# Performance work log

Measured on AMD Instinct MI355X. Metric: run time of the kernel, lower is better.

## Reference

```python
import jax, jax.numpy as jnp
import numpy as np

C = 345  # class_num


def setup_inputs() -> dict:
    key = jax.random.key(0)
    k1, k2, k3, k4, k5, k6, k7 = jax.random.split(key, 7)
    N, A = 128, 512
    fc_weight = jax.random.normal(k1, (C, A), dtype=jnp.float32) * 0.02
    features_source = jax.random.normal(k2, (N, A), dtype=jnp.float32)
    y_s = jax.random.normal(k3, (N, C), dtype=jnp.float32)
    labels_source = jax.random.randint(k4, (N,), 0, C, dtype=jnp.int64)
    mean_source = jax.random.normal(k5, (C, A), dtype=jnp.float32) * 0.1
    mean_target = jax.random.normal(k6, (C, A), dtype=jnp.float32) * 0.1
    covariance_target = jax.random.normal(k7, (C, A, A), dtype=jnp.float32) * 0.01
    Lambda = jnp.float32(0.5)
    return {
        "fc_weight": fc_weight,
        "features_source": features_source,
        "y_s": y_s,
        "labels_source": labels_source,
        "Lambda": Lambda,
        "mean_source": mean_source,
        "mean_target": mean_target,
        "covariance_target": covariance_target,
    }


def _aug(fc_weight, y_s, labels_s, Lambda, mean_source, mean_target, covariance_target):
    # NxW_ij = weight broadcast to [N,C,A]; NxW_kj = weight[labels] broadcast over C.
    # dataW[n,c,:] = W[c] - W[labels[n]]   -> [N,C,A]
    W_lbl = fc_weight[labels_s]                       # [N,A]
    dataW = fc_weight[None, :, :] - W_lbl[:, None, :]  # [N,C,A]

    Sigma = covariance_target[labels_s]               # [N,A,A]
    # diag of (dataW @ Sigma @ dataW^T): einsum directly for the diagonal
    tmp = jnp.einsum('nca,nab->ncb', dataW, Sigma)    # [N,C,A]
    sigma2 = Lambda * jnp.einsum('nca,nca->nc', tmp, dataW)  # [N,C]

    dMean = mean_target[labels_s] - mean_source[labels_s]   # [N,A]
    dW_dMean = jnp.einsum('nca,na->nc', dataW, dMean)        # [N,C]

    return y_s + 0.5 * sigma2 + Lambda * dW_dMean


def reference(fc_weight, features_source, y_s, labels_source, Lambda,
              mean_source, mean_target, covariance_target):
    aug_y = _aug(fc_weight, y_s, labels_source, Lambda,
                 mean_source, mean_target, covariance_target)
    logp = jax.nn.log_softmax(aug_y, axis=-1)
    N = aug_y.shape[0]
    nll = -logp[jnp.arange(N), labels_source]
    return jnp.mean(nll)
```

## Files before the change

kernel.cpp:

```cpp
#include <hip/hip_runtime.h>
#include <hip/hip_bf16.h>
#include <math.h>

#define C_NUM 345
#define A_DIM 512
#define N_NUM 128
#define KB    128
#define NBB   4

typedef short bf16x8 __attribute__((ext_vector_type(8)));
typedef float f32x4  __attribute__((ext_vector_type(4)));

__device__ __forceinline__ short f2bf(float f) {
    unsigned u = __builtin_bit_cast(unsigned, f);
    u += 0x7fffu + ((u >> 16) & 1u);
    return (short)(u >> 16);
}

__device__ __forceinline__ int swz(int r, int k) {
    return r * 128 + ((((k >> 3) ^ (r & 15)) << 3) | (k & 7));
}

__global__ __launch_bounds__(256, 2) void qkern(
    const float* __restrict__ W,
    const int*   __restrict__ labels,
    const float* __restrict__ cov,
    float*       __restrict__ q2)
{
    const int bb = blockIdx.x;
    const int n  = blockIdx.y;
    const int b0 = bb * KB;
    const int l  = labels[n];
    const float* __restrict__ Sg = cov + (size_t)l * A_DIM * A_DIM;
    const float* __restrict__ Wl = W + (size_t)l * A_DIM;

    __shared__ short Sa[128 * 128];
    __shared__ short Vb[128 * 128];

    const int tid  = threadIdx.x;
    const int lane = tid & 63;
    const int w    = tid >> 6;
    const int wa   = w & 1;
    const int wc   = w >> 1;
    const int l15  = lane & 15;
    const int g    = lane >> 4;

    const int c4 = tid & 31;
    const int r0 = tid >> 5;

    const float4 wl4 = *(const float4*)(Wl + b0 + c4 * 4);

    float qp[3][4];
#pragma unroll
    for (int ct = 0; ct < 3; ct++)
#pragma unroll
        for (int j = 0; j < 4; j++) qp[ct][j] = 0.f;

    for (int at = 0; at < A_DIM; at += 128) {
        float4 wle[4];
#pragma unroll
        for (int i = 0; i < 4; i++)
            wle[i] = *(const float4*)(Wl + at + wa * 64 + i * 16 + g * 4);

        for (int ct = 0; ct < 3; ct++) {
            __syncthreads();
            if (ct == 0) {
#pragma unroll
                for (int p = 0; p < 16; p++) {
                    const int r = r0 + p * 8;
                    const float4 s = *(const float4*)(Sg + (size_t)(at + r) * A_DIM + b0 + c4 * 4);
                    short4 h = make_short4(f2bf(s.x), f2bf(s.y), f2bf(s.z), f2bf(s.w));
                    *(short4*)(&Sa[swz(r, c4 * 4)]) = h;
                }
            }
#pragma unroll
            for (int p = 0; p < 16; p++) {
                const int r = r0 + p * 8;
                const int c = ct * 128 + r;
                short4 h;
                if (c < C_NUM) {
                    const float4 wv = *(const float4*)(W + (size_t)c * A_DIM + b0 + c4 * 4);
                    h = make_short4(f2bf(wv.x - wl4.x), f2bf(wv.y - wl4.y),
                                    f2bf(wv.z - wl4.z), f2bf(wv.w - wl4.w));
                } else {
                    h = make_short4(0, 0, 0, 0);
                }
                *(short4*)(&Vb[swz(r, c4 * 4)]) = h;
            }
            __syncthreads();

            f32x4 acc[4][4];
#pragma unroll
            for (int i = 0; i < 4; i++)
#pragma unroll
                for (int j = 0; j < 4; j++) {
                    f32x4 z = {0.f, 0.f, 0.f, 0.f};
                    acc[i][j] = z;
                }

#pragma unroll
            for (int kt = 0; kt < 4; kt++) {
                const int kbase = kt * 32 + g * 8;
                bf16x8 af[4], bfr[4];
#pragma unroll
                for (int i = 0; i < 4; i++)
                    af[i] = *(const bf16x8*)(&Sa[swz(wa * 64 + i * 16 + l15, kbase)]);
#pragma unroll
                for (int j = 0; j < 4; j++)
                    bfr[j] = *(const bf16x8*)(&Vb[swz(wc * 64 + j * 16 + l15, kbase)]);
#pragma unroll
                for (int i = 0; i < 4; i++)
#pragma unroll
                    for (int j = 0; j < 4; j++)
                        acc[i][j] = __builtin_amdgcn_mfma_f32_16x16x32_bf16(
                            af[i], bfr[j], acc[i][j], 0, 0, 0);
            }

#pragma unroll
            for (int i = 0; i < 4; i++) {
                const int a0 = at + wa * 64 + i * 16 + g * 4;
                const float4 wl_e = wle[i];
#pragma unroll
                for (int j = 0; j < 4; j++) {
                    const int c = ct * 128 + wc * 64 + j * 16 + l15;
                    if (c < C_NUM) {
                        const float4 wv = *(const float4*)(W + (size_t)c * A_DIM + a0);
                        const f32x4 u = acc[i][j];
                        qp[ct][j] += u[0] * (wv.x - wl_e.x) + u[1] * (wv.y - wl_e.y)
                                   + u[2] * (wv.z - wl_e.z) + u[3] * (wv.w - wl_e.w);
                    }
                }
            }
        }
    }

#pragma unroll
    for (int ct = 0; ct < 3; ct++)
#pragma unroll
        for (int j = 0; j < 4; j++) {
            float v = qp[ct][j];
            v += __shfl_xor(v, 16);
            v += __shfl_xor(v, 32);
            if (g == 0) {
                const int c = ct * 128 + wc * 64 + j * 16 + l15;
                if (c < C_NUM) atomicAdd(&q2[(size_t)n * C_NUM + c], v);
            }
        }
}

__global__ __launch_bounds__(256) void losskern(
    const float* __restrict__ W,
    const float* __restrict__ ys,
    const int*   __restrict__ labels,
    const float* __restrict__ lambda_p,
    const float* __restrict__ mean_s,
    const float* __restrict__ mean_t,
    const float* __restrict__ q2,
    float*       __restrict__ out)
{
    const int n = blockIdx.x;
    const int tid = threadIdx.x;
    const int lane = tid & 63;
    const int w = tid >> 6;
    const int l = labels[n];
    const float Lam = *lambda_p;

    __shared__ float aug[C_NUM];
    __shared__ float red[256];

    const int a0 = lane * 8;
    const float* Wl = W + (size_t)l * A_DIM;
    const float4 wl0 = *(const float4*)(Wl + a0);
    const float4 wl1 = *(const float4*)(Wl + a0 + 4);
    const float4 mt0 = *(const float4*)(mean_t + (size_t)l * A_DIM + a0);
    const float4 mt1 = *(const float4*)(mean_t + (size_t)l * A_DIM + a0 + 4);
    const float4 ms0 = *(const float4*)(mean_s + (size_t)l * A_DIM + a0);
    const float4 ms1 = *(const float4*)(mean_s + (size_t)l * A_DIM + a0 + 4);
    const float dm0 = mt0.x - ms0.x, dm1 = mt0.y - ms0.y, dm2 = mt0.z - ms0.z, dm3 = mt0.w - ms0.w;
    const float dm4 = mt1.x - ms1.x, dm5 = mt1.y - ms1.y, dm6 = mt1.z - ms1.z, dm7 = mt1.w - ms1.w;
    const float wldm = wl0.x*dm0 + wl0.y*dm1 + wl0.z*dm2 + wl0.w*dm3
                     + wl1.x*dm4 + wl1.y*dm5 + wl1.z*dm6 + wl1.w*dm7;

    for (int c = w; c < C_NUM; c += 4) {
        const float* Wc = W + (size_t)c * A_DIM;
        const float4 w0 = *(const float4*)(Wc + a0);
        const float4 w1 = *(const float4*)(Wc + a0 + 4);
        float d = w0.x*dm0 + w0.y*dm1 + w0.z*dm2 + w0.w*dm3
                + w1.x*dm4 + w1.y*dm5 + w1.z*dm6 + w1.w*dm7 - wldm;
        d += __shfl_xor(d, 1);
        d += __shfl_xor(d, 2);
        d += __shfl_xor(d, 4);
        d += __shfl_xor(d, 8);
        d += __shfl_xor(d, 16);
        d += __shfl_xor(d, 32);
        if (lane == 0)
            aug[c] = ys[(size_t)n * C_NUM + c] + 0.5f * Lam * q2[(size_t)n * C_NUM + c] + Lam * d;
    }
    __syncthreads();

    float m = -INFINITY;
    for (int c = tid; c < C_NUM; c += 256) m = fmaxf(m, aug[c]);
    red[tid] = m;
    __syncthreads();
    for (int s = 128; s > 0; s >>= 1) {
        if (tid < s) red[tid] = fmaxf(red[tid], red[tid + s]);
        __syncthreads();
    }
    m = red[0];
    __syncthreads();

    float se = 0.f;
    for (int c = tid; c < C_NUM; c += 256) se += expf(aug[c] - m);
    red[tid] = se;
    __syncthreads();
    for (int s = 128; s > 0; s >>= 1) {
        if (tid < s) red[tid] += red[tid + s];
        __syncthreads();
    }
    if (tid == 0) {
        const float logZ = m + logf(red[0]);
        atomicAdd(out, (logZ - aug[l]) * (1.f / (float)N_NUM));
    }
}

extern "C" void kernel_launch(void* const* d_in, const int* in_sizes, int n_in,
                              void* d_out, int out_size, void* d_ws, size_t ws_size,
                              hipStream_t stream) {
    const float* W      = (const float*)d_in[0];
    const float* ys     = (const float*)d_in[2];
    const int*   labels = (const int*)d_in[3];
    const float* lam    = (const float*)d_in[4];
    const float* means  = (const float*)d_in[5];
    const float* meant  = (const float*)d_in[6];
    const float* cov    = (const float*)d_in[7];
    float* out = (float*)d_out;
    float* q2  = (float*)d_ws;

    hipMemsetAsync(q2, 0, (size_t)N_NUM * C_NUM * sizeof(float), stream);
    hipMemsetAsync(out, 0, sizeof(float), stream);

    qkern<<<dim3(NBB, N_NUM), 256, 0, stream>>>(W, labels, cov, q2);
    losskern<<<N_NUM, 256, 0, stream>>>(W, ys, labels, lam, means, meant, q2, out);
}
```

Before: 555.2 us.

## Keep full W-difference tile resident in LDS and double-buffer covariance tiles

The quadratic-form kernel now uses 64-wide b-chunks over 8 blocks per sample. For each chunk it loads the whole padded 384-row weight-difference tile into shared memory once, instead of rebuilding it for every class tile and every a-tile. Covariance tiles are register-prefetched for the next a-step and written into a double-buffered shared array, so global loads overlap the MFMA work and only one barrier is needed per step. This removes repeated W conversions and cuts synchronisation. In exchange it doubles the grid and increases accumulator register pressure (4x6 MFMA tiles per wave).

After: 573.4 us. +3.3%, slower.

```diff
diff --git a/kernel.cpp b/kernel.cpp
--- a/kernel.cpp
+++ b/kernel.cpp
@@ -3,10 +3,11 @@
 #include <math.h>
 
 #define C_NUM 345
+#define CP    384
 #define A_DIM 512
 #define N_NUM 128
-#define KB    128
-#define NBB   4
+#define KB    64
+#define NBB   8
 
 typedef short bf16x8 __attribute__((ext_vector_type(8)));
 typedef float f32x4  __attribute__((ext_vector_type(4)));
@@ -17,8 +18,8 @@
     return (short)(u >> 16);
 }
 
-__device__ __forceinline__ int swz(int r, int k) {
-    return r * 128 + ((((k >> 3) ^ (r & 15)) << 3) | (k & 7));
+__device__ __forceinline__ int swz64(int r, int k) {
+    return r * 64 + ((((k >> 3) ^ (r & 7)) << 3) | (k & 7));
 }
 
 __global__ __launch_bounds__(256, 2) void qkern(
@@ -34,118 +35,120 @@
     const float* __restrict__ Sg = cov + (size_t)l * A_DIM * A_DIM;
     const float* __restrict__ Wl = W + (size_t)l * A_DIM;
 
-    __shared__ short Sa[128 * 128];
-    __shared__ short Vb[128 * 128];
+    __shared__ short Vb[CP * KB];
+    __shared__ short Sa[2][64 * KB];
 
     const int tid  = threadIdx.x;
     const int lane = tid & 63;
     const int w    = tid >> 6;
-    const int wa   = w & 1;
-    const int wc   = w >> 1;
     const int l15  = lane & 15;
     const int g    = lane >> 4;
 
-    const int c4 = tid & 31;
-    const int r0 = tid >> 5;
+    const int c4 = tid & 15;
+    const int r0 = tid >> 4;
+
+    float4 pf[4];
+    {
+        const float* sp = Sg + b0 + c4 * 4;
+#pragma unroll
+        for (int p = 0; p < 4; p++)
+            pf[p] = *(const float4*)(sp + (size_t)(r0 + p * 16) * A_DIM);
+    }
 
     const float4 wl4 = *(const float4*)(Wl + b0 + c4 * 4);
-
-    float qp[3][4];
-#pragma unroll
-    for (int ct = 0; ct < 3; ct++)
-#pragma unroll
-        for (int j = 0; j < 4; j++) qp[ct][j] = 0.f;
-
-    for (int at = 0; at < A_DIM; at += 128) {
-        float4 wle[4];
+#pragma unroll
+    for (int p = 0; p < 24; p++) {
+        const int r = r0 + p * 16;
+        short4 h = make_short4(0, 0, 0, 0);
+        if (r < C_NUM) {
+            const float4 wv = *(const float4*)(W + (size_t)r * A_DIM + b0 + c4 * 4);
+            h = make_short4(f2bf(wv.x - wl4.x), f2bf(wv.y - wl4.y),
+                            f2bf(wv.z - wl4.z), f2bf(wv.w - wl4.w));
+        }
+        *(short4*)(&Vb[swz64(r, c4 * 4)]) = h;
+    }
+#pragma unroll
+    for (int p = 0; p < 4; p++) {
+        const float4 s = pf[p];
+        *(short4*)(&Sa[0][swz64(r0 + p * 16, c4 * 4)]) =
+            make_short4(f2bf(s.x), f2bf(s.y), f2bf(s.z), f2bf(s.w));
+    }
+    __syncthreads();
+
+    float qp[6] = {0.f, 0.f, 0.f, 0.f, 0.f, 0.f};
+
+    for (int at = 0; at < 8; at++) {
+        if (at < 7) {
+            const float* sp = Sg + (size_t)(at + 1) * 64 * A_DIM + b0 + c4 * 4;
+#pragma unroll
+            for (int p = 0; p < 4; p++)
+                pf[p] = *(const float4*)(sp + (size_t)(r0 + p * 16) * A_DIM);
+        }
+
+        f32x4 acc[4][6];
 #pragma unroll
         for (int i = 0; i < 4; i++)
-            wle[i] = *(const float4*)(Wl + at + wa * 64 + i * 16 + g * 4);
-
-        for (int ct = 0; ct < 3; ct++) {
-            __syncthreads();
-            if (ct == 0) {
-#pragma unroll
-                for (int p = 0; p < 16; p++) {
-                    const int r = r0 + p * 8;
-                    const float4 s = *(const float4*)(Sg + (size_t)(at + r) * A_DIM + b0 + c4 * 4);
-                    short4 h = make_short4(f2bf(s.x), f2bf(s.y), f2bf(s.z), f2bf(s.w));
-                    *(short4*)(&Sa[swz(r, c4 * 4)]) = h;
+#pragma unroll
+            for (int j = 0; j < 6; j++) {
+                f32x4 z = {0.f, 0.f, 0.f, 0.f};
+                acc[i][j] = z;
+            }
+        const short* buf = Sa[at & 1];
+#pragma unroll
+        for (int kt = 0; kt < 2; kt++) {
+            const int kb = kt * 32 + g * 8;
+            bf16x8 af[4], bv[6];
+#pragma unroll
+            for (int i = 0; i < 4; i++)
+                af[i] = *(const bf16x8*)(&buf[swz64(i * 16 + l15, kb)]);
+#pragma unroll
+            for (int j = 0; j < 6; j++)
+                bv[j] = *(const bf16x8*)(&Vb[swz64(w * 96 + j * 16 + l15, kb)]);
+#pragma unroll
+            for (int i = 0; i < 4; i++)
+#pragma unroll
+                for (int j = 0; j < 6; j++)
+                    acc[i][j] = __builtin_amdgcn_mfma_f32_16x16x32_bf16(
+                        af[i], bv[j], acc[i][j], 0, 0, 0);
+        }
+
+#pragma unroll
+        for (int i = 0; i < 4; i++) {
+            const int a0 = at * 64 + i * 16 + g * 4;
+            const float4 wle = *(const float4*)(Wl + a0);
+#pragma unroll
+            for (int j = 0; j < 6; j++) {
+                const int c = w * 96 + j * 16 + l15;
+                if (c < C_NUM) {
+                    const float4 wv = *(const float4*)(W + (size_t)c * A_DIM + a0);
+                    const f32x4 u = acc[i][j];
+                    qp[j] += u[0] * (wv.x - wle.x) + u[1] * (wv.y - wle.y)
+                           + u[2] * (wv.z - wle.z) + u[3] * (wv.w - wle.w);
                 }
             }
-#pragma unroll
-            for (int p = 0; p < 16; p++) {
-                const int r = r0 + p * 8;
-                const int c = ct * 128 + r;
-                short4 h;
-                if (c < C_NUM) {
-                    const float4 wv = *(const float4*)(W + (size_t)c * A_DIM + b0 + c4 * 4);
-                    h = make_short4(f2bf(wv.x - wl4.x), f2bf(wv.y - wl4.y),
-                                    f2bf(wv.z - wl4.z), f2bf(wv.w - wl4.w));
-                } else {
-                    h = make_short4(0, 0, 0, 0);
-                }
-                *(short4*)(&Vb[swz(r, c4 * 4)]) = h;
+        }
+
+        if (at < 7) {
+#pragma unroll
+            for (int p = 0; p < 4; p++) {
+                const float4 s = pf[p];
+                *(short4*)(&Sa[(at + 1) & 1][swz64(r0 + p * 16, c4 * 4)]) =
+                    make_short4(f2bf(s.x), f2bf(s.y), f2bf(s.z), f2bf(s.w));
             }
-            __syncthreads();
-
-            f32x4 acc[4][4];
-#pragma unroll
-            for (int i = 0; i < 4; i++)
-#pragma unroll
-                for (int j = 0; j < 4; j++) {
-                    f32x4 z = {0.f, 0.f, 0.f, 0.f};
-                    acc[i][j] = z;
-                }
-
-#pragma unroll
-            for (int kt = 0; kt < 4; kt++) {
-                const int kbase = kt * 32 + g * 8;
-                bf16x8 af[4], bfr[4];
-#pragma unroll
-                for (int i = 0; i < 4; i++)
-                    af[i] = *(const bf16x8*)(&Sa[swz(wa * 64 + i * 16 + l15, kbase)]);
-#pragma unroll
-                for (int j = 0; j < 4; j++)
-                    bfr[j] = *(const bf16x8*)(&Vb[swz(wc * 64 + j * 16 + l15, kbase)]);
-#pragma unroll
-                for (int i = 0; i < 4; i++)
-#pragma unroll
-                    for (int j = 0; j < 4; j++)
-                        acc[i][j] = __builtin_amdgcn_mfma_f32_16x16x32_bf16(
-                            af[i], bfr[j], acc[i][j], 0, 0, 0);
-            }
-
-#pragma unroll
-            for (int i = 0; i < 4; i++) {
-                const int a0 = at + wa * 64 + i * 16 + g * 4;
-                const float4 wl_e = wle[i];
-#pragma unroll
-                for (int j = 0; j < 4; j++) {
-                    const int c = ct * 128 + wc * 64 + j * 16 + l15;
-                    if (c < C_NUM) {
-                        const float4 wv = *(const float4*)(W + (size_t)c * A_DIM + a0);
-                        const f32x4 u = acc[i][j];
-                        qp[ct][j] += u[0] * (wv.x - wl_e.x) + u[1] * (wv.y - wl_e.y)
-                                   + u[2] * (wv.z - wl_e.z) + u[3] * (wv.w - wl_e.w);
-                    }
-                }
-            }
-        }
-    }
-
-#pragma unroll
-    for (int ct = 0; ct < 3; ct++)
-#pragma unroll
-        for (int j = 0; j < 4; j++) {
-            float v = qp[ct][j];
-            v += __shfl_xor(v, 16);
-            v += __shfl_xor(v, 32);
-            if (g == 0) {
-                const int c = ct * 128 + wc * 64 + j * 16 + l15;
-                if (c < C_NUM) atomicAdd(&q2[(size_t)n * C_NUM + c], v);
-            }
-        }
+        }
+        __syncthreads();
+    }
+
+#pragma unroll
+    for (int j = 0; j < 6; j++) {
+        float v = qp[j];
+        v += __shfl_xor(v, 16);
+        v += __shfl_xor(v, 32);
+        if (g == 0) {
+            const int c = w * 96 + j * 16 + l15;
+            if (c < C_NUM) atomicAdd(&q2[(size_t)n * C_NUM + c], v);
+        }
+    }
 }
 
 __global__ __launch_bounds__(256) void losskern(
```
